# Performance work log

Hardware: AMD Instinct MI355X
Metric: run time of the kernel (lower is better)

Reference implementation:

```python
import jax, jax.numpy as jnp
import numpy as np

# --- SLAYER-style constants (network.yaml defaults) ---
T_BINS = 350      # tSample / Ts
TS = 1.0          # simulation time step
THETA = 10.0      # spike threshold
TAU_SR = 10.0     # SRM (psp) kernel time constant
TAU_REF = 1.0     # refractory kernel time constant
SCALE_REF = 2.0
TAU_RHO = 1.0     # surrogate-gradient width (unused in fwd)
SCALE_RHO = 1.0
REF_LEN = 32      # truncated refractory kernel length
B = 32            # batch

_t = jnp.arange(T_BINS, dtype=jnp.float32) * TS
SRM_KERNEL = (_t / TAU_SR) * jnp.exp(1.0 - _t / TAU_SR)            # alpha kernel, peak 1 at t=tauSr
_tr = jnp.arange(REF_LEN, dtype=jnp.float32) * TS
REF_KERNEL = -SCALE_REF * THETA * (_tr / TAU_REF) * jnp.exp(1.0 - _tr / TAU_REF)


def psp(x):
    # causal temporal convolution with SRM kernel; x: [B, N, T]
    b, n, t = x.shape
    k = SRM_KERNEL[::-1].reshape(1, 1, T_BINS)  # flip: lax conv is cross-correlation
    y = jax.lax.conv_general_dilated(x.reshape(b * n, 1, t), k, (1,), [(T_BINS - 1, 0)])
    return y.reshape(b, n, t)


def _spike_fwd_impl(u):
    # threshold + refractory dynamics, serial over time; u: [B, N, T]
    uT = jnp.moveaxis(u, -1, 0)  # [T, B, N]
    def step(buf, ut):
        v = ut + buf[..., 0]                       # membrane + pending refractory
        s = (v >= THETA).astype(u.dtype)           # 0/1 spike indicator
        buf = jnp.concatenate([buf[..., 1:], jnp.zeros_like(buf[..., :1])], axis=-1) \
              + s[..., None] * REF_KERNEL
        return buf, s / TS
    buf0 = jnp.zeros(u.shape[:-1] + (REF_LEN,), u.dtype)
    _, sT = jax.lax.scan(step, buf0, uT)
    return jnp.moveaxis(sT, 0, -1)


@jax.custom_vjp
def spike(u):
    return _spike_fwd_impl(u)

def _spike_f(u):
    return _spike_fwd_impl(u), u

def _spike_b(u, g):
    # SLAYER surrogate gradient: pdf of spiking
    pdf = (SCALE_RHO / TAU_RHO) * jnp.exp(-jnp.abs(u - THETA) / TAU_RHO)
    return (g * pdf,)

spike.defvjp(_spike_f, _spike_b)


def encode(inp, table):
    # vectorized pixel->time-bin one-hot scatter (replaces the Python quadruple loop)
    t_idx = table[inp]                                   # gather: [B,3,32,32]
    return jax.nn.one_hot(t_idx, T_BINS, dtype=jnp.float32) / TS  # [B,3,32,32,T]


def setup_inputs() -> dict:
    key = jax.random.key(0)
    k1, k2, k3 = jax.random.split(key, 3)
    inp = jax.random.randint(k1, (B, 3, 32, 32), 0, 256, dtype=jnp.int32)
    table = ((jnp.arange(256) * T_BINS) // 256).astype(jnp.int32)  # pixel value -> time bin
    w1 = jax.random.normal(k2, (240, 3 * 32 * 32), dtype=jnp.float32)
    w2 = jax.random.normal(k3, (10, 240), dtype=jnp.float32)
    return {"inp": inp, "table": table, "w1": w1, "w2": w2}


def reference(inp, table, w1, w2):
    spikes = encode(inp, table).reshape(inp.shape[0], -1, T_BINS)      # [B,3072,T]
    l1 = spike(psp(jnp.einsum('bpt,np->bnt', spikes, w1)))             # [B,240,T]
    l2 = spike(psp(jnp.einsum('bpt,np->bnt', l1, w2)))                 # [B,10,T]
    return l2
```

## Files before the change

### kernel.cpp

```cpp
#include <hip/hip_runtime.h>
#include <math.h>

#define T_BINS 350
#define REF_LEN 32
#define NB 32
#define NPIX 3072
#define N1 240
#define N2 10
#define NVAL 256

__global__ void prep(const int* __restrict__ inp,
                     int* __restrict__ pix,
                     int* __restrict__ offs,
                     int* __restrict__ cnts,
                     const float* __restrict__ w1,
                     float* __restrict__ w1t,
                     const int* __restrict__ table,
                     int* __restrict__ inv)
{
    __shared__ int lc[NVAL];
    __shared__ int ls[NVAL];
    __shared__ int lslot[NVAL];
    __shared__ float tile[64][65];
    __shared__ int linv[T_BINS];

    const int tid = threadIdx.x;

    if (blockIdx.x < NB) {
        const int b = blockIdx.x;
        lc[tid] = 0;
        __syncthreads();

        int vals[12];
        #pragma unroll
        for (int i = 0; i < 12; ++i) {
            int v = inp[b * NPIX + i * 256 + tid];
            vals[i] = v;
            atomicAdd(&lc[v], 1);
        }
        __syncthreads();

        int x = lc[tid];
        ls[tid] = x;
        __syncthreads();
        for (int d = 1; d < 256; d <<= 1) {
            int y = (tid >= d) ? ls[tid - d] : 0;
            __syncthreads();
            ls[tid] += y;
            __syncthreads();
        }
        int excl = ls[tid] - x;
        offs[b * NVAL + tid] = excl;
        cnts[b * NVAL + tid] = x;
        lslot[tid] = excl;
        __syncthreads();

        #pragma unroll
        for (int i = 0; i < 12; ++i) {
            int slot = atomicAdd(&lslot[vals[i]], 1);
            pix[b * NPIX + slot] = i * 256 + tid;
        }
    } else if (blockIdx.x < NB + 192) {
        const int tt = blockIdx.x - NB;
        const int p0 = (tt % 48) * 64;
        const int n0 = (tt / 48) * 64;
        const int c  = tid & 63;
        const int r0 = tid >> 6;

        #pragma unroll
        for (int i = 0; i < 16; ++i) {
            int n = n0 + r0 + i * 4;
            if (n < N1) tile[r0 + i * 4][c] = w1[n * NPIX + p0 + c];
        }
        __syncthreads();
        #pragma unroll
        for (int i = 0; i < 16; ++i) {
            int p = p0 + r0 + i * 4;
            int n = n0 + c;
            if (n < N1) w1t[p * N1 + n] = tile[c][r0 + i * 4];
        }
    } else {
        for (int i = tid; i < T_BINS; i += 256) linv[i] = -1;
        __syncthreads();
        if (tid < NVAL) linv[table[tid]] = tid;
        __syncthreads();
        for (int i = tid; i < T_BINS; i += 256) inv[i] = linv[i];
    }
}

__global__ void compute_u1(const float* __restrict__ w1t,
                           const int* __restrict__ pix,
                           const int* __restrict__ offs,
                           const int* __restrict__ cnts,
                           const int* __restrict__ inv,
                           float* __restrict__ u1t)
{
    const int t = blockIdx.x;
    const int b = blockIdx.y;
    const int tid = threadIdx.x;
    if (tid >= N1) return;
    const int v = inv[t];

    double acc = 0.0;
    if (v >= 0) {
        const int cnt = cnts[b * NVAL + v];
        const int* pl = pix + b * NPIX + offs[b * NVAL + v];
        int i = 0;
        for (; i + 4 <= cnt; i += 4) {
            int p0 = pl[i], p1 = pl[i + 1], p2 = pl[i + 2], p3 = pl[i + 3];
            double w0 = (double)w1t[p0 * N1 + tid];
            double w1v = (double)w1t[p1 * N1 + tid];
            double w2v = (double)w1t[p2 * N1 + tid];
            double w3 = (double)w1t[p3 * N1 + tid];
            acc += w0; acc += w1v; acc += w2v; acc += w3;
        }
        for (; i < cnt; ++i)
            acc += (double)w1t[pl[i] * N1 + tid];
    }
    u1t[((size_t)b * T_BINS + t) * N1 + tid] = (float)acc;
}

#define DYN_CONSTS \
    const double A    = 0.9048374180359595;     \
    const double C    = 0.2718281828459045;     \
    const double Ar   = 0.36787944117144233;    \
    const double Cr   = -54.365636569180904;    \
    const double C31A = 1.0671679036256927e-12; \
    const double C31B = 3.4424771084699765e-14;

#define DYN_CORE(uin)                                         \
        q = A * (q + p);                                      \
        p = A * p + (uin);                                    \
        double vm = C * q + Cr * Q;                           \
        unsigned int sb = (vm >= 10.0) ? 1u : 0u;             \
        double s = (double)sb;                                \
        double sel31 = (hist & 0x80000000u) ? C31A : 0.0;     \
        double sel30 = (hist & 0x40000000u) ? C31B : 0.0;     \
        Q = Ar * (Q + P - sel31);                             \
        P = s + (Ar * P - sel30);                             \
        hist = (hist << 1) | sb;

__global__ __launch_bounds__(64) void layer1_dyn(
                           const float* __restrict__ u1t,
                           unsigned long long* __restrict__ s1m)
{
    const int tid = threadIdx.x;
    const int b   = blockIdx.x >> 2;
    const int k   = blockIdx.x & 3;
    const int n   = k * 64 + tid;
    if (n >= N1) return;

    const float* ub = u1t + (size_t)b * T_BINS * N1 + n;
    unsigned long long* mp = s1m + ((size_t)b * T_BINS) * 4 + k;

    DYN_CONSTS
    double p = 0.0, q = 0.0, P = 0.0, Q = 0.0;
    unsigned int hist = 0u;

    double cb[14], nb[14];
    #pragma unroll
    for (int i = 0; i < 14; ++i) cb[i] = (double)ub[(size_t)i * N1];

    for (int t0 = 0; t0 < T_BINS; t0 += 14) {
        if (t0 + 14 < T_BINS) {
            #pragma unroll
            for (int i = 0; i < 14; ++i)
                nb[i] = (double)ub[(size_t)(t0 + 14 + i) * N1];
        }
        #pragma unroll
        for (int i = 0; i < 14; ++i) {
            DYN_CORE(cb[i])
            unsigned long long msk = __ballot(sb != 0u);
            if (tid == 0) mp[(size_t)(t0 + i) * 4] = msk;
        }
        #pragma unroll
        for (int i = 0; i < 14; ++i) cb[i] = nb[i];
    }
}

__global__ void compute_u2(const unsigned long long* __restrict__ s1m,
                           const float* __restrict__ w2,
                           float* __restrict__ u2)
{
    __shared__ float lw2[N2][N1];
    const int tid = threadIdx.x;
    for (int i = tid; i < N2 * N1; i += 256) lw2[i / N1][i % N1] = w2[i];
    __syncthreads();

    int id = blockIdx.x * 256 + tid;
    if (id >= NB * T_BINS * N2) return;
    int bt = id / N2;
    int m  = id - bt * N2;
    const unsigned long long* mp = s1m + (size_t)bt * 4;

    double acc = 0.0;
    #pragma unroll
    for (int kk = 0; kk < 4; ++kk) {
        unsigned long long msk = mp[kk];
        while (msk) {
            int j = __ffsll(msk) - 1;
            acc += (double)lw2[m][kk * 64 + j];
            msk &= msk - 1;
        }
    }
    u2[id] = (float)acc;
}

__global__ void layer2_dyn(const float* __restrict__ u2,
                           float* __restrict__ out)
{
    const int id = blockIdx.x * 64 + threadIdx.x;
    if (id >= NB * N2) return;
    const int b = id / N2;
    const int m = id - b * N2;
    const float* up = u2 + (size_t)b * T_BINS * N2 + m;
    float*       op = out + ((size_t)b * N2 + m) * T_BINS;

    DYN_CONSTS
    double p = 0.0, q = 0.0, P = 0.0, Q = 0.0;
    unsigned int hist = 0u;

    double cb[14], nb[14];
    #pragma unroll
    for (int i = 0; i < 14; ++i) cb[i] = (double)up[(size_t)i * N2];

    for (int t0 = 0; t0 < T_BINS; t0 += 14) {
        if (t0 + 14 < T_BINS) {
            #pragma unroll
            for (int i = 0; i < 14; ++i)
                nb[i] = (double)up[(size_t)(t0 + 14 + i) * N2];
        }
        #pragma unroll
        for (int i = 0; i < 14; ++i) {
            DYN_CORE(cb[i])
            op[t0 + i] = (float)s;
        }
        #pragma unroll
        for (int i = 0; i < 14; ++i) cb[i] = nb[i];
    }
}

extern "C" void kernel_launch(void* const* d_in, const int* in_sizes, int n_in,
                              void* d_out, int out_size, void* d_ws, size_t ws_size,
                              hipStream_t stream) {
    const int*   inp   = (const int*)d_in[0];
    const int*   table = (const int*)d_in[1];
    const float* w1    = (const float*)d_in[2];
    const float* w2    = (const float*)d_in[3];
    float* out = (float*)d_out;

    char* ws = (char*)d_ws;
    size_t off = 0;
    float* u1t = (float*)(ws + off);  off += (size_t)NB * T_BINS * N1 * 4;
    float* u2  = (float*)(ws + off);  off += (size_t)NB * T_BINS * N2 * 4;
    float* w1t = (float*)(ws + off);  off += (size_t)NPIX * N1 * 4;
    unsigned long long* s1m = (unsigned long long*)(ws + off);
    off += (size_t)NB * T_BINS * 4 * 8;
    int*   pix = (int*)(ws + off);    off += (size_t)NB * NPIX * 4;
    int*  offs = (int*)(ws + off);    off += (size_t)NB * NVAL * 4;
    int*  cnts = (int*)(ws + off);    off += (size_t)NB * NVAL * 4;
    int*   inv = (int*)(ws + off);    off += (size_t)T_BINS * 4;

    prep<<<NB + 192 + 1, 256, 0, stream>>>(inp, pix, offs, cnts, w1, w1t, table, inv);
    compute_u1<<<dim3(T_BINS, NB), 256, 0, stream>>>(w1t, pix, offs, cnts, inv, u1t);
    layer1_dyn<<<NB * 4, 64, 0, stream>>>(u1t, s1m);
    compute_u2<<<(NB * T_BINS * N2 + 255) / 256, 256, 0, stream>>>(s1m, w2, u2);
    layer2_dyn<<<(NB * N2 + 63) / 64, 64, 0, stream>>>(u2, out);
}
```

Measured before the change: 150.0 us.

## Fuse layer-1 input accumulation with spike dynamics via shared-memory staging

Merges compute_u1 and layer1_dyn into one kernel. Each block holds 4 wavefronts that compute the 64-neuron membrane input for two time segments into LDS, then one wavefront runs the serial threshold and refractory recurrence from LDS. This removes the u1t global round trip and one launch. In exchange, gather parallelism drops to 128 blocks, and three of the four waves sit idle during the serial phase.

```diff
diff --git a/kernel.cpp b/kernel.cpp
--- a/kernel.cpp
+++ b/kernel.cpp
@@ -8,6 +8,8 @@
 #define N1 240
 #define N2 10
 #define NVAL 256
+#define SEG1 182
+#define SEG2 168
 
 __global__ void prep(const int* __restrict__ inp,
                      int* __restrict__ pix,
@@ -86,38 +88,6 @@
         __syncthreads();
         for (int i = tid; i < T_BINS; i += 256) inv[i] = linv[i];
     }
-}
-
-__global__ void compute_u1(const float* __restrict__ w1t,
-                           const int* __restrict__ pix,
-                           const int* __restrict__ offs,
-                           const int* __restrict__ cnts,
-                           const int* __restrict__ inv,
-                           float* __restrict__ u1t)
-{
-    const int t = blockIdx.x;
-    const int b = blockIdx.y;
-    const int tid = threadIdx.x;
-    if (tid >= N1) return;
-    const int v = inv[t];
-
-    double acc = 0.0;
-    if (v >= 0) {
-        const int cnt = cnts[b * NVAL + v];
-        const int* pl = pix + b * NPIX + offs[b * NVAL + v];
-        int i = 0;
-        for (; i + 4 <= cnt; i += 4) {
-            int p0 = pl[i], p1 = pl[i + 1], p2 = pl[i + 2], p3 = pl[i + 3];
-            double w0 = (double)w1t[p0 * N1 + tid];
-            double w1v = (double)w1t[p1 * N1 + tid];
-            double w2v = (double)w1t[p2 * N1 + tid];
-            double w3 = (double)w1t[p3 * N1 + tid];
-            acc += w0; acc += w1v; acc += w2v; acc += w3;
-        }
-        for (; i < cnt; ++i)
-            acc += (double)w1t[pl[i] * N1 + tid];
-    }
-    u1t[((size_t)b * T_BINS + t) * N1 + tid] = (float)acc;
 }
 
 #define DYN_CONSTS \
@@ -140,41 +110,71 @@
         P = s + (Ar * P - sel30);                             \
         hist = (hist << 1) | sb;
 
-__global__ __launch_bounds__(64) void layer1_dyn(
-                           const float* __restrict__ u1t,
-                           unsigned long long* __restrict__ s1m)
-{
-    const int tid = threadIdx.x;
-    const int b   = blockIdx.x >> 2;
-    const int k   = blockIdx.x & 3;
-    const int n   = k * 64 + tid;
-    if (n >= N1) return;
-
-    const float* ub = u1t + (size_t)b * T_BINS * N1 + n;
-    unsigned long long* mp = s1m + ((size_t)b * T_BINS) * 4 + k;
+__global__ __launch_bounds__(256) void l1_fused(
+                     const float* __restrict__ w1t,
+                     const int* __restrict__ pix,
+                     const int* __restrict__ offs,
+                     const int* __restrict__ cnts,
+                     const int* __restrict__ inv,
+                     unsigned long long* __restrict__ s1m)
+{
+    __shared__ float lu1[SEG1 * 64];
+    const int tid  = threadIdx.x;
+    const int lane = tid & 63;
+    const int wv   = tid >> 6;
+    const int b    = blockIdx.x >> 2;
+    const int k    = blockIdx.x & 3;
+    const int n    = k * 64 + lane;
+    const int nn   = (n < N1) ? n : 0;
+    const bool valid = (n < N1);
+
+    unsigned long long* mp = s1m + (size_t)b * T_BINS * 4 + k;
 
     DYN_CONSTS
     double p = 0.0, q = 0.0, P = 0.0, Q = 0.0;
     unsigned int hist = 0u;
 
-    double cb[14], nb[14];
-    #pragma unroll
-    for (int i = 0; i < 14; ++i) cb[i] = (double)ub[(size_t)i * N1];
-
-    for (int t0 = 0; t0 < T_BINS; t0 += 14) {
-        if (t0 + 14 < T_BINS) {
-            #pragma unroll
-            for (int i = 0; i < 14; ++i)
-                nb[i] = (double)ub[(size_t)(t0 + 14 + i) * N1];
-        }
-        #pragma unroll
-        for (int i = 0; i < 14; ++i) {
-            DYN_CORE(cb[i])
-            unsigned long long msk = __ballot(sb != 0u);
-            if (tid == 0) mp[(size_t)(t0 + i) * 4] = msk;
-        }
-        #pragma unroll
-        for (int i = 0; i < 14; ++i) cb[i] = nb[i];
+    for (int seg = 0; seg < 2; ++seg) {
+        const int lo  = (seg == 0) ? 0 : SEG1;
+        const int len = (seg == 0) ? SEG1 : SEG2;
+
+        for (int t = lo + wv; t < lo + len; t += 4) {
+            const int v = inv[t];
+            double acc = 0.0;
+            if (v >= 0) {
+                const int cnt = cnts[b * NVAL + v];
+                const int* pl = pix + b * NPIX + offs[b * NVAL + v];
+                int i = 0;
+                for (; i + 4 <= cnt; i += 4) {
+                    int p0 = pl[i], p1 = pl[i + 1], p2 = pl[i + 2], p3 = pl[i + 3];
+                    double w0  = (double)w1t[p0 * N1 + nn];
+                    double w1v = (double)w1t[p1 * N1 + nn];
+                    double w2v = (double)w1t[p2 * N1 + nn];
+                    double w3  = (double)w1t[p3 * N1 + nn];
+                    acc += w0; acc += w1v; acc += w2v; acc += w3;
+                }
+                for (; i < cnt; ++i)
+                    acc += (double)w1t[pl[i] * N1 + nn];
+            }
+            lu1[(t - lo) * 64 + lane] = valid ? (float)acc : 0.0f;
+        }
+        __syncthreads();
+
+        if (wv == 0) {
+            for (int c = 0; c < len; c += 14) {
+                double cb[14];
+                #pragma unroll
+                for (int i = 0; i < 14; ++i)
+                    cb[i] = (double)lu1[(c + i) * 64 + lane];
+                #pragma unroll
+                for (int i = 0; i < 14; ++i) {
+                    DYN_CORE(cb[i])
+                    unsigned long long msk = __ballot(sb != 0u);
+                    if (lane == 0) mp[(size_t)(lo + c + i) * 4] = msk;
+                }
+            }
+        }
+        __syncthreads();
     }
 }
 
@@ -251,9 +251,8 @@
 
     char* ws = (char*)d_ws;
     size_t off = 0;
-    float* u1t = (float*)(ws + off);  off += (size_t)NB * T_BINS * N1 * 4;
+    float* w1t = (float*)(ws + off);  off += (size_t)NPIX * N1 * 4;
     float* u2  = (float*)(ws + off);  off += (size_t)NB * T_BINS * N2 * 4;
-    float* w1t = (float*)(ws + off);  off += (size_t)NPIX * N1 * 4;
     unsigned long long* s1m = (unsigned long long*)(ws + off);
     off += (size_t)NB * T_BINS * 4 * 8;
     int*   pix = (int*)(ws + off);    off += (size_t)NB * NPIX * 4;
@@ -262,8 +261,7 @@
     int*   inv = (int*)(ws + off);    off += (size_t)T_BINS * 4;
 
     prep<<<NB + 192 + 1, 256, 0, stream>>>(inp, pix, offs, cnts, w1, w1t, table, inv);
-    compute_u1<<<dim3(T_BINS, NB), 256, 0, stream>>>(w1t, pix, offs, cnts, inv, u1t);
-    layer1_dyn<<<NB * 4, 64, 0, stream>>>(u1t, s1m);
+    l1_fused<<<NB * 4, 256, 0, stream>>>(w1t, pix, offs, cnts, inv, s1m);
     compute_u2<<<(NB * T_BINS * N2 + 255) / 256, 256, 0, stream>>>(s1m, w2, u2);
     layer2_dyn<<<(NB * N2 + 63) / 64, 64, 0, stream>>>(u2, out);
 }
```

Measured after the change: 224.4 us. 49.6% more time.
